# Performance work log

Measured on AMD Instinct MI355X. Metric: run time of the kernel, lower is better.

## Reference

```python
import jax, jax.numpy as jnp
import numpy as np

D_MODEL = 1024
N_HEADS = 16
D_HEAD = D_MODEL // N_HEADS
D_FF = 4 * D_MODEL
EPS = 1e-5


def _layernorm(x, g, b):
    mu = jnp.mean(x, axis=-1, keepdims=True)
    var = jnp.var(x, axis=-1, keepdims=True)
    return (x - mu) * jax.lax.rsqrt(var + EPS) * g + b


def setup_inputs() -> dict:
    key = jax.random.key(0)
    ks = jax.random.split(key, 16)
    s_attn = 1.0 / np.sqrt(D_MODEL)
    s_ff1 = 1.0 / np.sqrt(D_MODEL)
    s_ff2 = 1.0 / np.sqrt(D_FF)
    inp = {
        'x': jax.random.normal(ks[0], (2, 2048, D_MODEL), dtype=jnp.float32),
        'Wq': jax.random.uniform(ks[1], (D_MODEL, D_MODEL), jnp.float32, -s_attn, s_attn),
        'bq': jax.random.uniform(ks[2], (D_MODEL,), jnp.float32, -s_attn, s_attn),
        'Wk': jax.random.uniform(ks[3], (D_MODEL, D_MODEL), jnp.float32, -s_attn, s_attn),
        'bk': jax.random.uniform(ks[4], (D_MODEL,), jnp.float32, -s_attn, s_attn),
        'Wv': jax.random.uniform(ks[5], (D_MODEL, D_MODEL), jnp.float32, -s_attn, s_attn),
        'bv': jax.random.uniform(ks[6], (D_MODEL,), jnp.float32, -s_attn, s_attn),
        'Wo': jax.random.uniform(ks[7], (D_MODEL, D_MODEL), jnp.float32, -s_attn, s_attn),
        'bo': jax.random.uniform(ks[8], (D_MODEL,), jnp.float32, -s_attn, s_attn),
        'W1': jax.random.uniform(ks[9], (D_MODEL, D_FF), jnp.float32, -s_ff1, s_ff1),
        'b1': jax.random.uniform(ks[10], (D_FF,), jnp.float32, -s_ff1, s_ff1),
        'W2': jax.random.uniform(ks[11], (D_FF, D_MODEL), jnp.float32, -s_ff2, s_ff2),
        'b2': jax.random.uniform(ks[12], (D_MODEL,), jnp.float32, -s_ff2, s_ff2),
        'ln1_g': jnp.ones((D_MODEL,), jnp.float32),
        'ln1_b': jnp.zeros((D_MODEL,), jnp.float32),
        'ln2_g': jnp.ones((D_MODEL,), jnp.float32),
        'ln2_b': jnp.zeros((D_MODEL,), jnp.float32),
    }
    return inp


def reference(x, Wq, bq, Wk, bk, Wv, bv, Wo, bo, W1, b1, W2, b2, ln1_g, ln1_b, ln2_g, ln2_b):
    B, T, D = x.shape
    scale = D_HEAD ** -0.5

    # pre-norm MHSA + residual
    h = _layernorm(x, ln1_g, ln1_b)
    def split(z):  # [B,T,D] -> [B,H,T,d_h]
        return z.reshape(B, T, N_HEADS, D_HEAD).transpose(0, 2, 1, 3)
    Q = split(h @ Wq + bq)
    K = split(h @ Wk + bk)
    V = split(h @ Wv + bv)
    scores = jnp.einsum('bhqd,bhkd->bhqk', Q, K) * scale  # [B,H,T,T]
    attn = jax.nn.softmax(scores, axis=-1)
    out = jnp.einsum('bhqk,bhkd->bhqd', attn, V)
    out = out.transpose(0, 2, 1, 3).reshape(B, T, D)
    x = x + (out @ Wo + bo)

    # pre-norm FFN + residual
    h = _layernorm(x, ln2_g, ln2_b)
    ff = jax.nn.gelu(h @ W1 + b1, approximate=False) @ W2 + b2
    return x + ff
```

## Files before the change

### kernel.cpp

```cpp
#include <hip/hip_runtime.h>
#include <math.h>

#define SEQ   2048
#define DM    1024
#define LDQKV 3072
#define MTOK  4096

typedef float  f32x4   __attribute__((ext_vector_type(4)));
typedef __bf16 bf16x8  __attribute__((ext_vector_type(8)));
typedef short  short8  __attribute__((ext_vector_type(8)));
typedef short  short4v __attribute__((ext_vector_type(4)));

__device__ __forceinline__ short f2bf(float f) {
  union { float f; unsigned u; } v; v.f = f;
  unsigned r = v.u + 0x7fffu + ((v.u >> 16) & 1u);
  return (short)(r >> 16);
}

__device__ __forceinline__ void gl_lds16(const void* g, void* l) {
  __builtin_amdgcn_global_load_lds(
      (const __attribute__((address_space(1))) void*)g,
      (__attribute__((address_space(3))) void*)l, 16, 0, 0);
}

__device__ __forceinline__ f32x4 mfma_bf16(bf16x8 a, bf16x8 b, f32x4 c) {
  return __builtin_amdgcn_mfma_f32_16x16x32_bf16(a, b, c, 0, 0, 0);
}

__global__ __launch_bounds__(256) void transpose_cast_k(
    const float* __restrict__ W, short* __restrict__ Wt, int K, int N)
{
  __shared__ float tile[32][33];
  const int n0 = blockIdx.x * 32, k0 = blockIdx.y * 32;
  const int tx = threadIdx.x & 31, ty = threadIdx.x >> 5;
#pragma unroll
  for (int i = 0; i < 4; i++)
    tile[ty + i * 8][tx] = W[(size_t)(k0 + ty + i * 8) * N + n0 + tx];
  __syncthreads();
#pragma unroll
  for (int i = 0; i < 4; i++)
    Wt[(size_t)(n0 + ty + i * 8) * K + k0 + tx] = f2bf(tile[tx][ty + i * 8]);
}

__global__ __launch_bounds__(256) void ln_k(
    const float* __restrict__ x, const float* __restrict__ g,
    const float* __restrict__ b, short* __restrict__ out)
{
  const int row = blockIdx.x;
  const int tid = threadIdx.x;
  const float4 v = ((const float4*)(x + (size_t)row * DM))[tid];
  float s  = v.x + v.y + v.z + v.w;
  float ss = v.x * v.x + v.y * v.y + v.z * v.z + v.w * v.w;
#pragma unroll
  for (int m = 32; m >= 1; m >>= 1) { s += __shfl_xor(s, m); ss += __shfl_xor(ss, m); }
  __shared__ float red[8];
  const int wid = tid >> 6;
  if ((tid & 63) == 0) { red[wid] = s; red[4 + wid] = ss; }
  __syncthreads();
  s  = red[0] + red[1] + red[2] + red[3];
  ss = red[4] + red[5] + red[6] + red[7];
  const float mu  = s * (1.f / DM);
  const float var = ss * (1.f / DM) - mu * mu;
  const float rs  = rsqrtf(var + 1e-5f);
  const float4 gv = ((const float4*)g)[tid];
  const float4 bv = ((const float4*)b)[tid];
  short4v o;
  o[0] = f2bf((v.x - mu) * rs * gv.x + bv.x);
  o[1] = f2bf((v.y - mu) * rs * gv.y + bv.y);
  o[2] = f2bf((v.z - mu) * rs * gv.z + bv.z);
  o[3] = f2bf((v.w - mu) * rs * gv.w + bv.w);
  *(short4v*)(out + (size_t)row * DM + tid * 4) = o;
}

__global__ __launch_bounds__(256) void concat_bias_k(
    const float* __restrict__ bq, const float* __restrict__ bk,
    const float* __restrict__ bv, float* __restrict__ o)
{
  int i = blockIdx.x * 256 + threadIdx.x;
  if (i < 3072) {
    float v = (i < 1024) ? bq[i] : (i < 2048 ? bk[i - 1024] : bv[i - 2048]);
    o[i] = v;
  }
}

__global__ __launch_bounds__(256) void vtrans_k(
    const short* __restrict__ V, short* __restrict__ Vt)
{
  const int b = blockIdx.z, h = blockIdx.y, t0 = blockIdx.x * 64;
  __shared__ short tile[64][72];
  const int tid = threadIdx.x;
  const int r = tid >> 2, c = (tid & 3) * 16;
  const short* src = V + (size_t)(b * SEQ + t0 + r) * LDQKV + h * 64 + c;
  *(short8*)&tile[r][c]     = *(const short8*)src;
  *(short8*)&tile[r][c + 8] = *(const short8*)(src + 8);
  __syncthreads();
  const int d = tid >> 2;
  short8 o0, o1;
#pragma unroll
  for (int k = 0; k < 8; k++) o0[k] = tile[c + k][d];
#pragma unroll
  for (int k = 0; k < 8; k++) o1[k] = tile[c + 8 + k][d];
  short* dst = Vt + (((size_t)(b * 16 + h) * 64) + d) * 2048 + t0 + c;
  *(short8*)dst       = o0;
  *(short8*)(dst + 8) = o1;
}

template <bool GELU_, bool RESID, bool OUTBF16>
__global__ __launch_bounds__(256) void gemm_bt(
    const short* __restrict__ A, const short* __restrict__ Bt,
    const float* __restrict__ bias, const float* __restrict__ resid,
    void* __restrict__ Cout, int M, int N, int K)
{
  __shared__ __align__(16) short Abuf[2][128 * 32];
  __shared__ __align__(16) short Bbuf[2][128 * 32];
  const int tid = threadIdx.x, lane = tid & 63, wid = tid >> 6;
  const int wr = wid >> 1, wc = wid & 1;
  const int bm = blockIdx.x * 128, bn = blockIdx.y * 128;

  f32x4 acc[4][4] = {};

  const int arow  = wid * 32 + (lane >> 2);
  const int acol8 = (lane & 3) * 8;
  const short* Ag0 = A  + (size_t)(bm + arow)      * K + acol8;
  const short* Ag1 = A  + (size_t)(bm + arow + 16) * K + acol8;
  const short* Bg0 = Bt + (size_t)(bn + arow)      * K + acol8;
  const short* Bg1 = Bt + (size_t)(bn + arow + 16) * K + acol8;

  const int l0 = (wid * 32) * 32, l1 = (wid * 32 + 16) * 32;

  gl_lds16(Ag0, &Abuf[0][l0]);
  gl_lds16(Ag1, &Abuf[0][l1]);
  gl_lds16(Bg0, &Bbuf[0][l0]);
  gl_lds16(Bg1, &Bbuf[0][l1]);
  __syncthreads();

  int cur = 0;
  for (int k0 = 32; k0 < K; k0 += 32) {
    const int nxt = cur ^ 1;
    gl_lds16(Ag0 + k0, &Abuf[nxt][l0]);
    gl_lds16(Ag1 + k0, &Abuf[nxt][l1]);
    gl_lds16(Bg0 + k0, &Bbuf[nxt][l0]);
    gl_lds16(Bg1 + k0, &Bbuf[nxt][l1]);

    bf16x8 a[4], b[4];
#pragma unroll
    for (int mi = 0; mi < 4; mi++)
      a[mi] = *(const bf16x8*)&Abuf[cur][(wr * 64 + mi * 16 + (lane & 15)) * 32 + (lane >> 4) * 8];
#pragma unroll
    for (int ni = 0; ni < 4; ni++)
      b[ni] = *(const bf16x8*)&Bbuf[cur][(wc * 64 + ni * 16 + (lane & 15)) * 32 + (lane >> 4) * 8];
#pragma unroll
    for (int mi = 0; mi < 4; mi++)
#pragma unroll
      for (int ni = 0; ni < 4; ni++)
        acc[mi][ni] = mfma_bf16(a[mi], b[ni], acc[mi][ni]);

    __syncthreads();
    cur = nxt;
  }

  {
    bf16x8 a[4], b[4];
#pragma unroll
    for (int mi = 0; mi < 4; mi++)
      a[mi] = *(const bf16x8*)&Abuf[cur][(wr * 64 + mi * 16 + (lane & 15)) * 32 + (lane >> 4) * 8];
#pragma unroll
    for (int ni = 0; ni < 4; ni++)
      b[ni] = *(const bf16x8*)&Bbuf[cur][(wc * 64 + ni * 16 + (lane & 15)) * 32 + (lane >> 4) * 8];
#pragma unroll
    for (int mi = 0; mi < 4; mi++)
#pragma unroll
      for (int ni = 0; ni < 4; ni++)
        acc[mi][ni] = mfma_bf16(a[mi], b[ni], acc[mi][ni]);
  }

#pragma unroll
  for (int mi = 0; mi < 4; mi++) {
#pragma unroll
    for (int ni = 0; ni < 4; ni++) {
      const int col = bn + wc * 64 + ni * 16 + (lane & 15);
      const float bs = bias[col];
#pragma unroll
      for (int j = 0; j < 4; j++) {
        const int row = bm + wr * 64 + mi * 16 + (lane >> 4) * 4 + j;
        float v = acc[mi][ni][j] + bs;
        if (GELU_) v = 0.5f * v * (1.0f + erff(v * 0.70710678118654752f));
        if (RESID) v += resid[(size_t)row * N + col];
        if (OUTBF16) ((short*)Cout)[(size_t)row * N + col] = f2bf(v);
        else         ((float*)Cout)[(size_t)row * N + col] = v;
      }
    }
  }
}

template <bool GELU_, bool RESID, bool OUTBF16>
__global__ __launch_bounds__(512) void gemm_bt8(
    const short* __restrict__ A, const short* __restrict__ Bt,
    const float* __restrict__ bias, const float* __restrict__ resid,
    void* __restrict__ Cout, int M, int N, int K)
{
  __shared__ __align__(16) short Ab[2][2][128 * 32];
  __shared__ __align__(16) short Bb[2][2][64 * 32];
  const int tid = threadIdx.x, lane = tid & 63, wid = tid >> 6;
  const int kg = wid >> 2, w2 = wid & 3;
  const int wr = w2 >> 1, wc = w2 & 1;
  const int bm = blockIdx.x * 128, bn = blockIdx.y * 64;

  f32x4 acc[4][2] = {};

  const int r_l = lane >> 2;
  const int c8  = (lane & 3) * 8;
  const short* Ag0 = A  + (size_t)(bm + w2 * 32 + r_l)      * K + c8;
  const short* Ag1 = A  + (size_t)(bm + w2 * 32 + 16 + r_l) * K + c8;
  const short* Bg0 = Bt + (size_t)(bn + w2 * 16 + r_l)      * K + c8;

  const int la0 = (w2 * 32) * 32, la1 = (w2 * 32 + 16) * 32, lb0 = (w2 * 16) * 32;
  const int kbase = kg * 32;

  gl_lds16(Ag0 + kbase, &Ab[kg][0][la0]);
  gl_lds16(Ag1 + kbase, &Ab[kg][0][la1]);
  gl_lds16(Bg0 + kbase, &Bb[kg][0][lb0]);
  __syncthreads();

  const int nsteps = K >> 6;
  int cur = 0;
  for (int i = 1; i < nsteps; ++i) {
    const int k0 = i * 64 + kbase;
    const int nxt = cur ^ 1;
    gl_lds16(Ag0 + k0, &Ab[kg][nxt][la0]);
    gl_lds16(Ag1 + k0, &Ab[kg][nxt][la1]);
    gl_lds16(Bg0 + k0, &Bb[kg][nxt][lb0]);

    bf16x8 a[4], b[2];
#pragma unroll
    for (int mi = 0; mi < 4; mi++)
      a[mi] = *(const bf16x8*)&Ab[kg][cur][(wr * 64 + mi * 16 + (lane & 15)) * 32 + (lane >> 4) * 8];
#pragma unroll
    for (int ni = 0; ni < 2; ni++)
      b[ni] = *(const bf16x8*)&Bb[kg][cur][(wc * 32 + ni * 16 + (lane & 15)) * 32 + (lane >> 4) * 8];
#pragma unroll
    for (int mi = 0; mi < 4; mi++)
#pragma unroll
      for (int ni = 0; ni < 2; ni++)
        acc[mi][ni] = mfma_bf16(a[mi], b[ni], acc[mi][ni]);

    __syncthreads();
    cur = nxt;
  }

  {
    bf16x8 a[4], b[2];
#pragma unroll
    for (int mi = 0; mi < 4; mi++)
      a[mi] = *(const bf16x8*)&Ab[kg][cur][(wr * 64 + mi * 16 + (lane & 15)) * 32 + (lane >> 4) * 8];
#pragma unroll
    for (int ni = 0; ni < 2; ni++)
      b[ni] = *(const bf16x8*)&Bb[kg][cur][(wc * 32 + ni * 16 + (lane & 15)) * 32 + (lane >> 4) * 8];
#pragma unroll
    for (int mi = 0; mi < 4; mi++)
#pragma unroll
      for (int ni = 0; ni < 2; ni++)
        acc[mi][ni] = mfma_bf16(a[mi], b[ni], acc[mi][ni]);
  }

  __syncthreads();

  float* red = (float*)&Ab[0][0][0];
  const int slot = (w2 * 64 + lane) * 8;
  if (kg == 1) {
#pragma unroll
    for (int mi = 0; mi < 4; mi++)
#pragma unroll
      for (int ni = 0; ni < 2; ni++)
        *(f32x4*)&red[(slot + mi * 2 + ni) * 4] = acc[mi][ni];
  }
  __syncthreads();
  if (kg == 0) {
#pragma unroll
    for (int mi = 0; mi < 4; mi++)
#pragma unroll
      for (int ni = 0; ni < 2; ni++)
        acc[mi][ni] += *(const f32x4*)&red[(slot + mi * 2 + ni) * 4];

#pragma unroll
    for (int mi = 0; mi < 4; mi++) {
#pragma unroll
      for (int ni = 0; ni < 2; ni++) {
        const int col = bn + wc * 32 + ni * 16 + (lane & 15);
        const float bs = bias[col];
#pragma unroll
        for (int j = 0; j < 4; j++) {
          const int row = bm + wr * 64 + mi * 16 + (lane >> 4) * 4 + j;
          float v = acc[mi][ni][j] + bs;
          if (GELU_) v = 0.5f * v * (1.0f + erff(v * 0.70710678118654752f));
          if (RESID) v += resid[(size_t)row * N + col];
          if (OUTBF16) ((short*)Cout)[(size_t)row * N + col] = f2bf(v);
          else         ((float*)Cout)[(size_t)row * N + col] = v;
        }
      }
    }
  }
}

__global__ __launch_bounds__(256) void attn_k(
    const short* __restrict__ Qg, const short* __restrict__ Kg,
    const short* __restrict__ Vt, short* __restrict__ Og)
{
  const int b = blockIdx.z, h = blockIdx.y, q0 = blockIdx.x * 64;
  const int tid = threadIdx.x, lane = tid & 63, w = tid >> 6;
  const int qlane = lane & 15, g = lane >> 4;

  __shared__ __align__(16) short Kl[128 * 64];
  __shared__ __align__(16) short Vl[64 * 128];

  char* KbC = (char*)Kl;
  char* VbC = (char*)Vl;

  const size_t qrow = (size_t)(b * SEQ + q0 + w * 16 + qlane) * LDQKV + h * 64;
  const bf16x8 qf0 = *(const bf16x8*)&Qg[qrow + g * 8];
  const bf16x8 qf1 = *(const bf16x8*)&Qg[qrow + 32 + g * 8];

  const int kslot = (lane & 7) ^ ((lane >> 3) & 7);
  const short* Kg_a[4];
#pragma unroll
  for (int i = 0; i < 4; i++) {
    const int r  = i * 32 + w * 8 + (lane >> 3);
    const int kc = r >> 4, gr = (r >> 2) & 3, jr = r & 3;
    const int a  = 32 * (kc & 3) + 8 * gr + 4 * (kc >> 2) + jr;
    Kg_a[i] = Kg + ((size_t)(b * SEQ) + a) * LDQKV + h * 64 + kslot * 8;
  }
  const short* Vt_head = Vt + ((size_t)(b * 16 + h) * 64) * 2048;

  float m_run = -1e30f, l_run = 0.f;
  f32x4 oacc[4] = {};
  const float C = 0.125f * 1.44269504088896f;

  for (int kt = 0; kt < SEQ; kt += 128) {
#pragma unroll
    for (int i = 0; i < 4; i++)
      gl_lds16(Kg_a[i] + (size_t)kt * LDQKV, &Kl[(i * 32 + w * 8) * 64]);
#pragma unroll
    for (int i = 0; i < 4; i++) {
      const int dloc = i * 4 + (lane >> 4);
      const int vs = (lane & 15) ^ dloc;
      gl_lds16(Vt_head + (size_t)(w * 16 + dloc) * 2048 + kt + vs * 8,
               &Vl[(w * 16 + i * 4) * 128]);
    }
    __syncthreads();

    f32x4 s[8];
#pragma unroll
    for (int kc = 0; kc < 8; kc++) {
      const int kr = kc * 16 + qlane;
      const char* kp = KbC + kr * 128;
      const int sw = (kr & 7) << 4;
      bf16x8 kf0 = *(const bf16x8*)(kp + ((g * 16) ^ sw));
      bf16x8 kf1 = *(const bf16x8*)(kp + ((64 + g * 16) ^ sw));
      f32x4 z = {};
      z = mfma_bf16(kf0, qf0, z);
      z = mfma_bf16(kf1, qf1, z);
      s[kc] = z;
    }

    f32x4 m4 = s[0];
#pragma unroll
    for (int kc = 1; kc < 8; kc++) {
      m4[0] = fmaxf(m4[0], s[kc][0]); m4[1] = fmaxf(m4[1], s[kc][1]);
      m4[2] = fmaxf(m4[2], s[kc][2]); m4[3] = fmaxf(m4[3], s[kc][3]);
    }
    float mt = fmaxf(fmaxf(m4[0], m4[1]), fmaxf(m4[2], m4[3]));
    mt = fmaxf(mt, __shfl_xor(mt, 16));
    mt = fmaxf(mt, __shfl_xor(mt, 32));

    if (!__all(mt - m_run <= 40.0f)) {
      const float mnew = fmaxf(m_run, mt);
      const float r = exp2f((m_run - mnew) * C);
      m_run = mnew;
      l_run *= r;
#pragma unroll
      for (int j = 0; j < 4; j++) {
        const float rj = __shfl(r, g * 4 + j);
#pragma unroll
        for (int dt = 0; dt < 4; dt++) oacc[dt][j] *= rj;
      }
    }

    const float nmc = -m_run * C;
    float rs = 0.f;
    unsigned pw[4][4];
#pragma unroll
    for (int kc = 0; kc < 8; kc++) {
      f32x4 p;
#pragma unroll
      for (int j = 0; j < 4; j++) p[j] = exp2f(fmaf(s[kc][j], C, nmc));
      rs += (p[0] + p[1]) + (p[2] + p[3]);
      unsigned w0, w1;
      asm("v_cvt_pk_bf16_f32 %0, %1, %2" : "=v"(w0) : "v"(p[0]), "v"(p[1]));
      asm("v_cvt_pk_bf16_f32 %0, %1, %2" : "=v"(w1) : "v"(p[2]), "v"(p[3]));
      pw[kc & 3][2 * (kc >> 2) + 0] = w0;
      pw[kc & 3][2 * (kc >> 2) + 1] = w1;
    }
    rs += __shfl_xor(rs, 16);
    rs += __shfl_xor(rs, 32);
    l_run += rs;

#pragma unroll
    for (int ks = 0; ks < 4; ks++) {
      union { unsigned u[4]; bf16x8 v; } pf;
      pf.u[0] = pw[ks][0]; pf.u[1] = pw[ks][1];
      pf.u[2] = pw[ks][2]; pf.u[3] = pw[ks][3];
#pragma unroll
      for (int dt = 0; dt < 4; dt++) {
        const int vr = dt * 16 + qlane;
        bf16x8 vf = *(const bf16x8*)(VbC + vr * 256 + ((64 * ks + 16 * g) ^ ((vr & 15) << 4)));
        oacc[dt] = mfma_bf16(pf.v, vf, oacc[dt]);
      }
    }
    __syncthreads();
  }

  const float linv = 1.f / l_run;
#pragma unroll
  for (int j = 0; j < 4; j++) {
    const float lj = __shfl(linv, g * 4 + j);
    const int tok = q0 + w * 16 + g * 4 + j;
#pragma unroll
    for (int dt = 0; dt < 4; dt++)
      Og[(size_t)(b * SEQ + tok) * DM + h * 64 + dt * 16 + qlane] = f2bf(oacc[dt][j] * lj);
  }
}

extern "C" void kernel_launch(void* const* d_in, const int* in_sizes, int n_in,
                              void* d_out, int out_size, void* d_ws, size_t ws_size,
                              hipStream_t stream)
{
  const float* x    = (const float*)d_in[0];
  const float* Wq   = (const float*)d_in[1];
  const float* bq   = (const float*)d_in[2];
  const float* Wk   = (const float*)d_in[3];
  const float* bk   = (const float*)d_in[4];
  const float* Wv   = (const float*)d_in[5];
  const float* bv   = (const float*)d_in[6];
  const float* Wo   = (const float*)d_in[7];
  const float* bo   = (const float*)d_in[8];
  const float* W1   = (const float*)d_in[9];
  const float* b1   = (const float*)d_in[10];
  const float* W2   = (const float*)d_in[11];
  const float* b2   = (const float*)d_in[12];
  const float* ln1g = (const float*)d_in[13];
  const float* ln1b = (const float*)d_in[14];
  const float* ln2g = (const float*)d_in[15];
  const float* ln2b = (const float*)d_in[16];

  char* ws = (char*)d_ws;
  const size_t MB = 1024 * 1024;
  short* Wqkvt = (short*)(ws + 0 * MB);
  short* Wqt   = Wqkvt;
  short* Wkt   = (short*)(ws + 2 * MB);
  short* Wvt   = (short*)(ws + 4 * MB);
  short* Wot   = (short*)(ws + 6 * MB);
  short* W1t   = (short*)(ws + 8 * MB);
  short* W2t   = (short*)(ws + 16 * MB);
  short* hbuf  = (short*)(ws + 24 * MB);
  short* QKV   = (short*)(ws + 32 * MB);
  short* AO    = (short*)(ws + 56 * MB);
  float* x1    = (float*)(ws + 64 * MB);
  short* Vtb   = (short*)(ws + 64 * MB);
  float* bqkv  = (float*)(ws + 80 * MB);
  short* gbuf  = (short*)(ws + 32 * MB);

  dim3 tb(256);

  transpose_cast_k<<<dim3(32, 32),  tb, 0, stream>>>(Wq, Wqt, 1024, 1024);
  transpose_cast_k<<<dim3(32, 32),  tb, 0, stream>>>(Wk, Wkt, 1024, 1024);
  transpose_cast_k<<<dim3(32, 32),  tb, 0, stream>>>(Wv, Wvt, 1024, 1024);
  transpose_cast_k<<<dim3(32, 32),  tb, 0, stream>>>(Wo, Wot, 1024, 1024);
  transpose_cast_k<<<dim3(128, 32), tb, 0, stream>>>(W1, W1t, 1024, 4096);
  transpose_cast_k<<<dim3(32, 128), tb, 0, stream>>>(W2, W2t, 4096, 1024);
  concat_bias_k<<<dim3(12), tb, 0, stream>>>(bq, bk, bv, bqkv);

  ln_k<<<dim3(MTOK), tb, 0, stream>>>(x, ln1g, ln1b, hbuf);

  gemm_bt<false, false, true><<<dim3(32, 24), tb, 0, stream>>>(
      hbuf, Wqkvt, bqkv, nullptr, QKV, MTOK, 3072, 1024);

  vtrans_k<<<dim3(32, 16, 2), tb, 0, stream>>>(QKV + 2048, Vtb);

  attn_k<<<dim3(32, 16, 2), tb, 0, stream>>>(QKV, QKV + 1024, Vtb, AO);

  gemm_bt8<false, true, false><<<dim3(32, 16), dim3(512), 0, stream>>>(
      AO, Wot, bo, x, x1, MTOK, 1024, 1024);

  ln_k<<<dim3(MTOK), tb, 0, stream>>>(x1, ln2g, ln2b, hbuf);

  gemm_bt<true, false, true><<<dim3(32, 32), tb, 0, stream>>>(
      hbuf, W1t, b1, nullptr, gbuf, MTOK, 4096, 1024);

  gemm_bt8<false, true, false><<<dim3(32, 16), dim3(512), 0, stream>>>(
      gbuf, W2t, b2, x1, (float*)d_out, MTOK, 1024, 4096);
}
```

Before: 304.1 us.

## Double-buffer K tiles, load V directly to registers, remap blocks for XCD locality

The attention kernel now double-buffers the K tile in LDS, prefetching the next tile while computing the current one. V is no longer staged through LDS; each lane loads its bf16x8 V fragments straight from global memory into registers, interleaved with the PV MFMAs. Block indices are remapped so that neighbouring blocks, which share K/V for a head, land on the same XCD, and launch bounds request 3 blocks per SM. The max reduction is also rebalanced into a shallower tree. The risks are higher register pressure and global-load latency exposed on V, since those loads bypass LDS and depend on cache hits.

```diff
diff --git a/kernel.cpp b/kernel.cpp
--- a/kernel.cpp
+++ b/kernel.cpp
@@ -302,19 +302,20 @@
   }
 }
 
-__global__ __launch_bounds__(256) void attn_k(
+__global__ __launch_bounds__(256, 3) void attn_k(
     const short* __restrict__ Qg, const short* __restrict__ Kg,
     const short* __restrict__ Vt, short* __restrict__ Og)
 {
-  const int b = blockIdx.z, h = blockIdx.y, q0 = blockIdx.x * 64;
+  const int phys = blockIdx.x + 32 * blockIdx.y + 512 * blockIdx.z;
+  const int lg   = (phys & 7) * 128 + (phys >> 3);
+  const int q0 = (lg & 31) * 64;
+  const int h  = (lg >> 5) & 15;
+  const int b  = lg >> 9;
+
   const int tid = threadIdx.x, lane = tid & 63, w = tid >> 6;
   const int qlane = lane & 15, g = lane >> 4;
 
-  __shared__ __align__(16) short Kl[128 * 64];
-  __shared__ __align__(16) short Vl[64 * 128];
-
-  char* KbC = (char*)Kl;
-  char* VbC = (char*)Vl;
+  __shared__ __align__(16) short Kl[2][128 * 64];
 
   const size_t qrow = (size_t)(b * SEQ + q0 + w * 16 + qlane) * LDQKV + h * 64;
   const bf16x8 qf0 = *(const bf16x8*)&Qg[qrow + g * 8];
@@ -329,24 +330,30 @@
     const int a  = 32 * (kc & 3) + 8 * gr + 4 * (kc >> 2) + jr;
     Kg_a[i] = Kg + ((size_t)(b * SEQ) + a) * LDQKV + h * 64 + kslot * 8;
   }
-  const short* Vt_head = Vt + ((size_t)(b * 16 + h) * 64) * 2048;
+
+  const short* Vrow[4];
+#pragma unroll
+  for (int dt = 0; dt < 4; dt++)
+    Vrow[dt] = Vt + ((size_t)(b * 16 + h) * 64 + dt * 16 + qlane) * 2048 + 8 * g;
 
   float m_run = -1e30f, l_run = 0.f;
   f32x4 oacc[4] = {};
   const float C = 0.125f * 1.44269504088896f;
 
+#pragma unroll
+  for (int i = 0; i < 4; i++)
+    gl_lds16(Kg_a[i], &Kl[0][(i * 32 + w * 8) * 64]);
+  __syncthreads();
+
+  int cur = 0;
   for (int kt = 0; kt < SEQ; kt += 128) {
-#pragma unroll
-    for (int i = 0; i < 4; i++)
-      gl_lds16(Kg_a[i] + (size_t)kt * LDQKV, &Kl[(i * 32 + w * 8) * 64]);
-#pragma unroll
-    for (int i = 0; i < 4; i++) {
-      const int dloc = i * 4 + (lane >> 4);
-      const int vs = (lane & 15) ^ dloc;
-      gl_lds16(Vt_head + (size_t)(w * 16 + dloc) * 2048 + kt + vs * 8,
-               &Vl[(w * 16 + i * 4) * 128]);
-    }
-    __syncthreads();
+    const int nxt = cur ^ 1;
+    if (kt + 128 < SEQ) {
+#pragma unroll
+      for (int i = 0; i < 4; i++)
+        gl_lds16(Kg_a[i] + (size_t)(kt + 128) * LDQKV, &Kl[nxt][(i * 32 + w * 8) * 64]);
+    }
+    const char* KbC = (const char*)&Kl[cur][0];
 
     f32x4 s[8];
 #pragma unroll
@@ -362,13 +369,22 @@
       s[kc] = z;
     }
 
-    f32x4 m4 = s[0];
-#pragma unroll
-    for (int kc = 1; kc < 8; kc++) {
-      m4[0] = fmaxf(m4[0], s[kc][0]); m4[1] = fmaxf(m4[1], s[kc][1]);
-      m4[2] = fmaxf(m4[2], s[kc][2]); m4[3] = fmaxf(m4[3], s[kc][3]);
-    }
-    float mt = fmaxf(fmaxf(m4[0], m4[1]), fmaxf(m4[2], m4[3]));
+    bf16x8 vfa[4], vfb[4];
+#pragma unroll
+    for (int dt = 0; dt < 4; dt++) vfa[dt] = *(const bf16x8*)(Vrow[dt] + kt);
+#pragma unroll
+    for (int dt = 0; dt < 4; dt++) vfb[dt] = *(const bf16x8*)(Vrow[dt] + kt + 32);
+
+    f32x4 t0 = s[0], t1 = s[3], t2 = s[6];
+#pragma unroll
+    for (int c4 = 0; c4 < 4; c4++) {
+      t0[c4] = fmaxf(fmaxf(t0[c4], s[1][c4]), s[2][c4]);
+      t1[c4] = fmaxf(fmaxf(t1[c4], s[4][c4]), s[5][c4]);
+      t2[c4] = fmaxf(t2[c4], s[7][c4]);
+    }
+    float mt = fmaxf(fmaxf(fmaxf(t0[0], t0[1]), fmaxf(t0[2], t0[3])),
+                     fmaxf(fmaxf(fmaxf(t1[0], t1[1]), fmaxf(t1[2], t1[3])),
+                           fmaxf(fmaxf(t2[0], t2[1]), fmaxf(t2[2], t2[3]))));
     mt = fmaxf(mt, __shfl_xor(mt, 16));
     mt = fmaxf(mt, __shfl_xor(mt, 32));
 
@@ -404,19 +420,26 @@
     rs += __shfl_xor(rs, 32);
     l_run += rs;
 
-#pragma unroll
-    for (int ks = 0; ks < 4; ks++) {
-      union { unsigned u[4]; bf16x8 v; } pf;
-      pf.u[0] = pw[ks][0]; pf.u[1] = pw[ks][1];
-      pf.u[2] = pw[ks][2]; pf.u[3] = pw[ks][3];
-#pragma unroll
-      for (int dt = 0; dt < 4; dt++) {
-        const int vr = dt * 16 + qlane;
-        bf16x8 vf = *(const bf16x8*)(VbC + vr * 256 + ((64 * ks + 16 * g) ^ ((vr & 15) << 4)));
-        oacc[dt] = mfma_bf16(pf.v, vf, oacc[dt]);
-      }
-    }
+    union { unsigned u[4]; bf16x8 v; } pf;
+    pf.u[0] = pw[0][0]; pf.u[1] = pw[0][1]; pf.u[2] = pw[0][2]; pf.u[3] = pw[0][3];
+#pragma unroll
+    for (int dt = 0; dt < 4; dt++) oacc[dt] = mfma_bf16(pf.v, vfa[dt], oacc[dt]);
+#pragma unroll
+    for (int dt = 0; dt < 4; dt++) vfa[dt] = *(const bf16x8*)(Vrow[dt] + kt + 64);
+    pf.u[0] = pw[1][0]; pf.u[1] = pw[1][1]; pf.u[2] = pw[1][2]; pf.u[3] = pw[1][3];
+#pragma unroll
+    for (int dt = 0; dt < 4; dt++) oacc[dt] = mfma_bf16(pf.v, vfb[dt], oacc[dt]);
+#pragma unroll
+    for (int dt = 0; dt < 4; dt++) vfb[dt] = *(const bf16x8*)(Vrow[dt] + kt + 96);
+    pf.u[0] = pw[2][0]; pf.u[1] = pw[2][1]; pf.u[2] = pw[2][2]; pf.u[3] = pw[2][3];
+#pragma unroll
+    for (int dt = 0; dt < 4; dt++) oacc[dt] = mfma_bf16(pf.v, vfa[dt], oacc[dt]);
+    pf.u[0] = pw[3][0]; pf.u[1] = pw[3][1]; pf.u[2] = pw[3][2]; pf.u[3] = pw[3][3];
+#pragma unroll
+    for (int dt = 0; dt < 4; dt++) oacc[dt] = mfma_bf16(pf.v, vfb[dt], oacc[dt]);
+
     __syncthreads();
+    cur = nxt;
   }
 
   const float linv = 1.f / l_run;
```

Result: slower. 354.6 us (+16.6%).

## Double-buffer K/V tiles in attention, widen blocks to 128 queries, remap grid

Applied to the files above, without the earlier changes.

The attention kernel now keeps two LDS buffers for the K and V tiles and issues the async global-to-LDS loads for the next tile before computing on the current one. This is meant to hide load latency behind the MFMA work. Blocks grow to 512 threads covering 128 queries, so each K/V tile is shared by twice as many query rows. The grid becomes a swizzled 1D mapping of 512 blocks. The costs are double the LDS per block (64KB), half as many blocks, and only one barrier per iteration, which could race if the prefetch into the next buffer overlaps reads of the old one.

```diff
diff --git a/kernel.cpp b/kernel.cpp
--- a/kernel.cpp
+++ b/kernel.cpp
@@ -302,51 +302,66 @@
   }
 }
 
-__global__ __launch_bounds__(256) void attn_k(
+__global__ __launch_bounds__(512, 4) void attn_k(
     const short* __restrict__ Qg, const short* __restrict__ Kg,
     const short* __restrict__ Vt, short* __restrict__ Og)
 {
-  const int b = blockIdx.z, h = blockIdx.y, q0 = blockIdx.x * 64;
+  const int phys = blockIdx.x;
+  const int lg = (phys & 7) * 64 + (phys >> 3);
+  const int q0 = (lg & 15) * 128;
+  const int h  = (lg >> 4) & 15;
+  const int b  = lg >> 8;
+
   const int tid = threadIdx.x, lane = tid & 63, w = tid >> 6;
   const int qlane = lane & 15, g = lane >> 4;
 
-  __shared__ __align__(16) short Kl[128 * 64];
-  __shared__ __align__(16) short Vl[64 * 128];
-
-  char* KbC = (char*)Kl;
-  char* VbC = (char*)Vl;
+  __shared__ __align__(16) short Kl[2][128 * 64];
+  __shared__ __align__(16) short Vl[2][64 * 128];
 
   const size_t qrow = (size_t)(b * SEQ + q0 + w * 16 + qlane) * LDQKV + h * 64;
   const bf16x8 qf0 = *(const bf16x8*)&Qg[qrow + g * 8];
   const bf16x8 qf1 = *(const bf16x8*)&Qg[qrow + 32 + g * 8];
 
   const int kslot = (lane & 7) ^ ((lane >> 3) & 7);
-  const short* Kg_a[4];
-#pragma unroll
-  for (int i = 0; i < 4; i++) {
-    const int r  = i * 32 + w * 8 + (lane >> 3);
+  const short* Kg_a[2];
+#pragma unroll
+  for (int i = 0; i < 2; i++) {
+    const int r  = i * 64 + w * 8 + (lane >> 3);
     const int kc = r >> 4, gr = (r >> 2) & 3, jr = r & 3;
     const int a  = 32 * (kc & 3) + 8 * gr + 4 * (kc >> 2) + jr;
     Kg_a[i] = Kg + ((size_t)(b * SEQ) + a) * LDQKV + h * 64 + kslot * 8;
   }
-  const short* Vt_head = Vt + ((size_t)(b * 16 + h) * 64) * 2048;
+  const short* Vg_s[2];
+#pragma unroll
+  for (int i = 0; i < 2; i++) {
+    const int d  = i * 32 + w * 4 + (lane >> 4);
+    const int vs = (lane & 15) ^ (d & 15);
+    Vg_s[i] = Vt + ((size_t)(b * 16 + h) * 64 + d) * 2048 + vs * 8;
+  }
 
   float m_run = -1e30f, l_run = 0.f;
   f32x4 oacc[4] = {};
   const float C = 0.125f * 1.44269504088896f;
 
+#pragma unroll
+  for (int i = 0; i < 2; i++) {
+    gl_lds16(Kg_a[i], &Kl[0][(i * 64 + w * 8) * 64]);
+    gl_lds16(Vg_s[i], &Vl[0][(i * 32 + w * 4) * 128]);
+  }
+  __syncthreads();
+
+  int cur = 0;
   for (int kt = 0; kt < SEQ; kt += 128) {
-#pragma unroll
-    for (int i = 0; i < 4; i++)
-      gl_lds16(Kg_a[i] + (size_t)kt * LDQKV, &Kl[(i * 32 + w * 8) * 64]);
-#pragma unroll
-    for (int i = 0; i < 4; i++) {
-      const int dloc = i * 4 + (lane >> 4);
-      const int vs = (lane & 15) ^ dloc;
-      gl_lds16(Vt_head + (size_t)(w * 16 + dloc) * 2048 + kt + vs * 8,
-               &Vl[(w * 16 + i * 4) * 128]);
-    }
-    __syncthreads();
+    const int nxt = cur ^ 1;
+    if (kt + 128 < SEQ) {
+#pragma unroll
+      for (int i = 0; i < 2; i++) {
+        gl_lds16(Kg_a[i] + (size_t)(kt + 128) * LDQKV, &Kl[nxt][(i * 64 + w * 8) * 64]);
+        gl_lds16(Vg_s[i] + (kt + 128),                 &Vl[nxt][(i * 32 + w * 4) * 128]);
+      }
+    }
+    const char* KbC = (const char*)&Kl[cur][0];
+    const char* VbC = (const char*)&Vl[cur][0];
 
     f32x4 s[8];
 #pragma unroll
@@ -416,7 +431,9 @@
         oacc[dt] = mfma_bf16(pf.v, vf, oacc[dt]);
       }
     }
+
     __syncthreads();
+    cur = nxt;
   }
 
   const float linv = 1.f / l_run;
@@ -486,7 +503,7 @@
 
   vtrans_k<<<dim3(32, 16, 2), tb, 0, stream>>>(QKV + 2048, Vtb);
 
-  attn_k<<<dim3(32, 16, 2), tb, 0, stream>>>(QKV, QKV + 1024, Vtb, AO);
+  attn_k<<<dim3(512), dim3(512), 0, stream>>>(QKV, QKV + 1024, Vtb, AO);
 
   gemm_bt8<false, true, false><<<dim3(32, 16), dim3(512), 0, stream>>>(
       AO, Wot, bo, x, x1, MTOK, 1024, 1024);
```

After: 294.5 us. 1.03x faster.
